# Kernel tuning notes

Measured on AMD Instinct MI355X. Metric: run time of the kernel, lower is better.

The kernel has to match this reference:

```python
import jax, jax.numpy as jnp
import numpy as np

D_MODEL = 1024
N_HEADS = 16
HEAD_DIM = D_MODEL // N_HEADS
ROPE_BASE = 10000.0


def setup_inputs() -> dict:
    key = jax.random.key(0)
    ks = jax.random.split(key, 5)
    B, S = 4, 2048
    bound_qkv = 1.0 / np.sqrt(D_MODEL)
    bound_out = 1.0 / np.sqrt(D_MODEL)
    return {
        "query": jax.random.normal(ks[0], (B, S, D_MODEL), dtype=jnp.float32),
        "W_qkv": jax.random.uniform(ks[1], (3 * D_MODEL, D_MODEL), jnp.float32, -bound_qkv, bound_qkv),
        "b_qkv": jax.random.uniform(ks[2], (3 * D_MODEL,), jnp.float32, -bound_qkv, bound_qkv),
        "W_out": jax.random.uniform(ks[3], (D_MODEL, D_MODEL), jnp.float32, -bound_out, bound_out),
        "b_out": jax.random.uniform(ks[4], (D_MODEL,), jnp.float32, -bound_out, bound_out),
    }


def _rope(x):
    # x: [B, H, S, Dh]; rotate-half RoPE, full rotational fraction
    S, Dh = x.shape[2], x.shape[3]
    half = Dh // 2
    inv_freq = 1.0 / (ROPE_BASE ** (jnp.arange(0, half, dtype=jnp.float32) * 2.0 / Dh))
    ang = jnp.arange(S, dtype=jnp.float32)[:, None] * inv_freq[None, :]  # [S, half]
    cos = jnp.concatenate([jnp.cos(ang), jnp.cos(ang)], axis=-1)  # [S, Dh]
    sin = jnp.concatenate([jnp.sin(ang), jnp.sin(ang)], axis=-1)
    x1, x2 = x[..., :half], x[..., half:]
    rot = jnp.concatenate([-x2, x1], axis=-1)
    return x * cos + rot * sin


def reference(query, W_qkv, b_qkv, W_out, b_out):
    B, S, _ = query.shape
    qkv = query @ W_qkv.T + b_qkv  # [B, S, 3*D]
    qkv = qkv.reshape(B, S, 3, N_HEADS, HEAD_DIM).transpose(2, 0, 3, 1, 4)  # [3, B, H, S, Dh]
    q, k, v = qkv[0], qkv[1], qkv[2]
    q = _rope(q)
    k = _rope(k)
    scale = 1.0 / np.sqrt(HEAD_DIM)
    scores = jnp.einsum("bhsd,bhtd->bhst", q, k) * scale  # [B, H, S, S]
    attn = jax.nn.softmax(scores, axis=-1)
    out = jnp.einsum("bhst,bhtd->bhsd", attn, v)  # [B, H, S, Dh]
    out = out.transpose(0, 2, 1, 3).reshape(B, S, D_MODEL)
    return out @ W_out.T + b_out
```

## Files before the change

kernel.cpp:

```cpp
#include <hip/hip_runtime.h>
#include <math.h>

#define D_MODEL 1024
#define N_HEADS 16
#define HEAD_DIM 64
#define BATCH 4
#define SEQ 2048
#define TOKENS (BATCH * SEQ)

typedef _Float16 f16;
typedef f16 f16x8_t __attribute__((ext_vector_type(8)));
typedef f16 f16x4_t __attribute__((ext_vector_type(4)));
typedef float f32x4_t __attribute__((ext_vector_type(4)));

#define QSCALE 0.18033688011112042f

__device__ __forceinline__ void stage16(const f16* g, f16* l) {
    __builtin_amdgcn_global_load_lds(
        (__attribute__((address_space(1))) void*)g,
        (__attribute__((address_space(3))) void*)l, 16, 0, 0);
}

__global__ void rope_table_kernel(float* __restrict__ cosT, float* __restrict__ sinT) {
    int idx = blockIdx.x * blockDim.x + threadIdx.x;
    int s = idx >> 5;
    int i = idx & 31;
    double t = (double)(2 * i) / 64.0;
    double invf = pow(10000.0, -t);
    double ang = (double)s * invf;
    cosT[idx] = (float)cos(ang);
    sinT[idx] = (float)sin(ang);
}

#define N_X  (TOKENS * D_MODEL / 4)
#define N_WQ (3 * D_MODEL * D_MODEL / 4)
#define N_WO (D_MODEL * D_MODEL / 4)
__global__ void convert_all_kernel(const float* __restrict__ X,
                                   const float* __restrict__ Wq,
                                   const float* __restrict__ Wo,
                                   f16* __restrict__ Xf, f16* __restrict__ Wqf,
                                   f16* __restrict__ Wof) {
    int i = blockIdx.x * blockDim.x + threadIdx.x;
    const float* src;
    f16* dst;
    int j;
    if (i < N_X)             { src = X;  dst = Xf;  j = i; }
    else if (i < N_X + N_WQ) { src = Wq; dst = Wqf; j = i - N_X; }
    else                     { src = Wo; dst = Wof; j = i - N_X - N_WQ; }
    float4 x = ((const float4*)src)[j];
    f16x4_t h;
    h[0] = (f16)x.x; h[1] = (f16)x.y; h[2] = (f16)x.z; h[3] = (f16)x.w;
    ((f16x4_t*)dst)[j] = h;
}

__device__ __forceinline__ void gemm_mainloop(
    const f16* __restrict__ A, const f16* __restrict__ B,
    int n0, int c0, f16* As, f16* Bs, f32x4_t acc[4][4]) {
    const int tid = threadIdx.x;
    const int lane = tid & 63;
    const int wave = tid >> 6;
    const int m16 = lane & 15, quad = lane >> 4;
    const int wm = (wave & 1) * 64, wn = (wave >> 1) * 64;

    const int srow = lane >> 3;
    const int scol = (lane & 7) << 3;

#pragma unroll
    for (int i = 0; i < 4; i++)
#pragma unroll
        for (int j = 0; j < 4; j++) acc[i][j] = (f32x4_t){0.f, 0.f, 0.f, 0.f};

    f16* ldsA = As + (wave * 32) * 64;
    f16* ldsB = Bs + (wave * 32) * 64;
    const f16* ga = A + (size_t)(n0 + wave * 32 + srow) * D_MODEL + scol;
    const f16* gb = B + (size_t)(c0 + wave * 32 + srow) * D_MODEL + scol;

    for (int kt = 0; kt < 16; kt++) {
        const int ko = kt * 64;
        __syncthreads();
#pragma unroll
        for (int inst = 0; inst < 4; inst++) {
            stage16(ga + ko + (size_t)(inst * 8) * D_MODEL, ldsA + inst * 8 * 64);
            stage16(gb + ko + (size_t)(inst * 8) * D_MODEL, ldsB + inst * 8 * 64);
        }
        __syncthreads();
#pragma unroll
        for (int kk = 0; kk < 2; kk++) {
            f16x8_t a[4], b[4];
#pragma unroll
            for (int mt = 0; mt < 4; mt++)
                a[mt] = *(const f16x8_t*)&As[(wm + mt * 16 + m16) * 64 + kk * 32 + quad * 8];
#pragma unroll
            for (int nt = 0; nt < 4; nt++)
                b[nt] = *(const f16x8_t*)&Bs[(wn + nt * 16 + m16) * 64 + kk * 32 + quad * 8];
#pragma unroll
            for (int mt = 0; mt < 4; mt++)
#pragma unroll
                for (int nt = 0; nt < 4; nt++)
                    acc[mt][nt] = __builtin_amdgcn_mfma_f32_16x16x32_f16(
                        a[mt], b[nt], acc[mt][nt], 0, 0, 0);
        }
    }
}

__global__ __launch_bounds__(256)
void qkv_gemm_kernel(const f16* __restrict__ Xf, const f16* __restrict__ Wf,
                     const float* __restrict__ bias,
                     f16* __restrict__ Qb, f16* __restrict__ Kb,
                     f16* __restrict__ VbT,
                     const float* __restrict__ cosT, const float* __restrict__ sinT) {
    __shared__ f16 As[128 * 64];
    __shared__ f16 Bs[128 * 64];
    f32x4_t acc[4][4];
    const int n0 = blockIdx.y * 128;
    const int c0 = blockIdx.x * 128;
    gemm_mainloop(Xf, Wf, n0, c0, As, Bs, acc);

    const int lane = threadIdx.x & 63;
    const int wave = threadIdx.x >> 6;
    const int m16 = lane & 15, quad = lane >> 4;
    const int wm = (wave & 1) * 64, wn = (wave >> 1) * 64;

    const int w = c0 >> 10;
    const int hh = ((c0 + wn) & 1023) >> 6;
    const int b = n0 >> 11;

    float bias4[4];
#pragma unroll
    for (int nt = 0; nt < 4; nt++) bias4[nt] = bias[c0 + wn + nt * 16 + m16];

    if (w == 2) {
        f16* vbase = VbT + ((size_t)(b * N_HEADS + hh) * HEAD_DIM) * SEQ;
#pragma unroll
        for (int mt = 0; mt < 4; mt++) {
            const int sb = (n0 + wm + mt * 16 + quad * 4) & (SEQ - 1);
#pragma unroll
            for (int nt = 0; nt < 4; nt++) {
                const int dh = nt * 16 + m16;
                f16x4_t v4;
#pragma unroll
                for (int i = 0; i < 4; i++) v4[i] = (f16)(acc[mt][nt][i] + bias4[nt]);
                *(f16x4_t*)&vbase[(size_t)dh * SEQ + sb] = v4;
            }
        }
        return;
    }

    f16* dst = (w == 0) ? Qb : Kb;
#pragma unroll
    for (int mt = 0; mt < 4; mt++)
#pragma unroll
        for (int i = 0; i < 4; i++) {
            const int n = n0 + wm + mt * 16 + quad * 4 + i;
            const int s = n & (SEQ - 1);
            f16* drow = dst + ((size_t)(b * N_HEADS + hh) * SEQ + s) * HEAD_DIM;
            float vv[4];
#pragma unroll
            for (int nt = 0; nt < 4; nt++) vv[nt] = acc[mt][nt][i] + bias4[nt];
            const float cs0 = cosT[(s << 5) + m16];
            const float sn0 = sinT[(s << 5) + m16];
            const float cs1 = cosT[(s << 5) + 16 + m16];
            const float sn1 = sinT[(s << 5) + 16 + m16];
#pragma unroll
            for (int nt = 0; nt < 4; nt++) {
                const int dh = nt * 16 + m16;
                const float cs = (nt & 1) ? cs1 : cs0;
                const float sn = (nt & 1) ? sn1 : sn0;
                const float part = vv[nt ^ 2];
                float outv = (nt >= 2) ? fmaf(vv[nt], cs, part * sn)
                                       : fmaf(vv[nt], cs, -part * sn);
                if (w == 0) outv *= QSCALE;
                drow[dh] = (f16)outv;
            }
        }
}

__global__ __launch_bounds__(256)
void out_gemm_kernel(const f16* __restrict__ Of, const f16* __restrict__ Wf,
                     const float* __restrict__ bias, float* __restrict__ Cout) {
    __shared__ f16 As[128 * 64];
    __shared__ f16 Bs[128 * 64];
    f32x4_t acc[4][4];
    const int n0 = blockIdx.y * 128;
    const int c0 = blockIdx.x * 128;
    gemm_mainloop(Of, Wf, n0, c0, As, Bs, acc);

    const int lane = threadIdx.x & 63;
    const int wave = threadIdx.x >> 6;
    const int m16 = lane & 15, quad = lane >> 4;
    const int wm = (wave & 1) * 64, wn = (wave >> 1) * 64;

    float bias4[4];
#pragma unroll
    for (int nt = 0; nt < 4; nt++) bias4[nt] = bias[c0 + wn + nt * 16 + m16];

#pragma unroll
    for (int mt = 0; mt < 4; mt++)
#pragma unroll
        for (int i = 0; i < 4; i++) {
            const int n = n0 + wm + mt * 16 + quad * 4 + i;
            float* orow = Cout + (size_t)n * D_MODEL + c0 + wn;
#pragma unroll
            for (int nt = 0; nt < 4; nt++)
                orow[nt * 16 + m16] = acc[mt][nt][i] + bias4[nt];
        }
}

#define KSW(row, g) ((g) ^ ((row) & 7))
__global__ __launch_bounds__(256, 2)
void attn_kernel(const f16* __restrict__ Qb, const f16* __restrict__ Kb,
                 const f16* __restrict__ VbT, f16* __restrict__ Of) {
    __shared__ f16 Ks[64 * 64];
    __shared__ f16 Vs[64 * 64];
    __shared__ f16 Ps[4][64][72];

    const int tid  = threadIdx.x;
    const int lane = tid & 63;
    const int wave = tid >> 6;
    const int m16  = lane & 15;
    const int quad = lane >> 4;

    const int bh = blockIdx.x & 63;
    const int qt = blockIdx.x >> 6;
    const int s0 = qt * 256;

    const f16* Kbase  = Kb + (size_t)bh * SEQ * HEAD_DIM;
    const f16* VtBase = VbT + (size_t)bh * HEAD_DIM * SEQ;

    f16x8_t bq[4][2];
#pragma unroll
    for (int nq = 0; nq < 4; nq++) {
        const f16* qrow = Qb + ((size_t)bh * SEQ + s0 + wave * 64 + nq * 16 + m16)
                          * HEAD_DIM + quad * 8;
        bq[nq][0] = *(const f16x8_t*)(qrow);
        bq[nq][1] = *(const f16x8_t*)(qrow + 32);
    }

    f32x4_t Oc[4][4];
#pragma unroll
    for (int mt = 0; mt < 4; mt++)
#pragma unroll
        for (int nq = 0; nq < 4; nq++) Oc[mt][nq] = (f32x4_t){0.f, 0.f, 0.f, 0.f};
    float sumacc[4] = {0.f, 0.f, 0.f, 0.f};

    const int lrow0 = wave * 16 + (lane >> 3);
    const int lrow1 = lrow0 + 8;
    const int gK0 = lrow0 * HEAD_DIM + KSW(lrow0, lane & 7) * 8;
    const int gK1 = lrow1 * HEAD_DIM + KSW(lrow1, lane & 7) * 8;
    const int gV0 = lrow0 * SEQ + KSW(lrow0, lane & 7) * 8;
    const int gV1 = lrow1 * SEQ + KSW(lrow1, lane & 7) * 8;
    f16* ldsK0 = Ks + (wave * 16) * 64;
    f16* ldsK1 = Ks + (wave * 16 + 8) * 64;
    f16* ldsV0 = Vs + (wave * 16) * 64;
    f16* ldsV1 = Vs + (wave * 16 + 8) * 64;

    for (int kt = 0; kt < SEQ / 64; kt++) {
        __syncthreads();
        const f16* kg = Kbase + (size_t)kt * 64 * HEAD_DIM;
        const f16* vg = VtBase + kt * 64;
        stage16(kg + gK0, ldsK0);
        stage16(kg + gK1, ldsK1);
        stage16(vg + gV0, ldsV0);
        stage16(vg + gV1, ldsV1);
        __syncthreads();

        f32x4_t Sc[4][4];
#pragma unroll
        for (int nt = 0; nt < 4; nt++)
#pragma unroll
            for (int nq = 0; nq < 4; nq++) Sc[nt][nq] = (f32x4_t){0.f, 0.f, 0.f, 0.f};
#pragma unroll
        for (int kki = 0; kki < 2; kki++) {
#pragma unroll
            for (int nt = 0; nt < 4; nt++) {
                const int row = nt * 16 + m16;
                f16x8_t ak = *(const f16x8_t*)&Ks[row * 64 + KSW(row, kki * 4 + quad) * 8];
#pragma unroll
                for (int nq = 0; nq < 4; nq++)
                    Sc[nt][nq] = __builtin_amdgcn_mfma_f32_16x16x32_f16(
                        ak, bq[nq][kki], Sc[nt][nq], 0, 0, 0);
            }
        }

#pragma unroll
        for (int nt = 0; nt < 4; nt++)
#pragma unroll
            for (int nq = 0; nq < 4; nq++) {
                f16x4_t pk4;
#pragma unroll
                for (int i = 0; i < 4; i++) {
                    float p = __builtin_amdgcn_exp2f(Sc[nt][nq][i]);
                    sumacc[nq] += p;
                    pk4[i] = (f16)p;
                }
                *(f16x4_t*)&Ps[wave][nq * 16 + m16][nt * 16 + quad * 4] = pk4;
            }

#pragma unroll
        for (int kki = 0; kki < 2; kki++) {
            f16x8_t bp[4];
#pragma unroll
            for (int nq = 0; nq < 4; nq++)
                bp[nq] = *(const f16x8_t*)&Ps[wave][nq * 16 + m16][kki * 32 + quad * 8];
#pragma unroll
            for (int mt = 0; mt < 4; mt++) {
                const int d = mt * 16 + m16;
                f16x8_t av = *(const f16x8_t*)&Vs[d * 64 + KSW(d, kki * 4 + quad) * 8];
#pragma unroll
                for (int nq = 0; nq < 4; nq++)
                    Oc[mt][nq] = __builtin_amdgcn_mfma_f32_16x16x32_f16(
                        av, bp[nq], Oc[mt][nq], 0, 0, 0);
            }
        }
    }

    const int b = bh >> 4, h = bh & 15;
#pragma unroll
    for (int nq = 0; nq < 4; nq++) {
        float l = sumacc[nq];
        l += __shfl_xor(l, 16);
        l += __shfl_xor(l, 32);
        const float invl = 1.0f / l;
        const int s = s0 + wave * 64 + nq * 16 + m16;
        const size_t off = ((size_t)(b * SEQ + s)) * D_MODEL + h * HEAD_DIM;
#pragma unroll
        for (int mt = 0; mt < 4; mt++) {
            f16x4_t o4;
#pragma unroll
            for (int i = 0; i < 4; i++)
                o4[i] = (f16)(Oc[mt][nq][i] * invl);
            *(f16x4_t*)&Of[off + mt * 16 + quad * 4] = o4;
        }
    }
}

extern "C" void kernel_launch(void* const* d_in, const int* in_sizes, int n_in,
                              void* d_out, int out_size, void* d_ws, size_t ws_size,
                              hipStream_t stream) {
    const float* X    = (const float*)d_in[0];
    const float* Wqkv = (const float*)d_in[1];
    const float* bqkv = (const float*)d_in[2];
    const float* Wout = (const float*)d_in[3];
    const float* bout = (const float*)d_in[4];
    float* out = (float*)d_out;

    char* w8 = (char*)d_ws;
    const size_t MB = 1024 * 1024;
    f16* Xf  = (f16*)(w8);
    f16* Wqf = (f16*)(w8 + 16 * MB);
    f16* Wof = (f16*)(w8 + 22 * MB);
    f16* Qf  = (f16*)(w8 + 24 * MB);
    f16* Kf  = (f16*)(w8 + 40 * MB);
    f16* VfT = (f16*)(w8 + 56 * MB);
    f16* Of  = (f16*)(w8 + 72 * MB);
    float* cosT = (float*)(w8 + 88 * MB);
    float* sinT = cosT + SEQ * 32;

    rope_table_kernel<<<(SEQ * 32) / 256, 256, 0, stream>>>(cosT, sinT);
    convert_all_kernel<<<(N_X + N_WQ + N_WO) / 256, 256, 0, stream>>>(
        X, Wqkv, Wout, Xf, Wqf, Wof);

    qkv_gemm_kernel<<<dim3(3 * D_MODEL / 128, TOKENS / 128), 256, 0, stream>>>(
        Xf, Wqf, bqkv, Qf, Kf, VfT, cosT, sinT);
    attn_kernel<<<64 * (SEQ / 256), 256, 0, stream>>>(Qf, Kf, VfT, Of);
    out_gemm_kernel<<<dim3(D_MODEL / 128, TOKENS / 128), 256, 0, stream>>>(
        Of, Wof, bout, out);
}
```

Measured before the change: 295.8 us.

## Double-buffer K/V tiles in attention and merge rope table into prep kernel

The attention kernel now keeps two K/V LDS buffers and issues the async global-to-LDS loads for the next tile before computing on the current one. This replaces the two barriers per iteration with one waitcnt plus barrier at the end of the loop. MFMA groups are wrapped in s_setprio to favour matrix issue. The rope table generation is folded into the conversion kernel to save a launch. The cost is doubled K/V LDS, which may reduce occupancy at two blocks per CU.

```diff
diff --git a/kernel.cpp b/kernel.cpp
--- a/kernel.cpp
+++ b/kernel.cpp
@@ -21,26 +21,28 @@
         (__attribute__((address_space(3))) void*)l, 16, 0, 0);
 }
 
-__global__ void rope_table_kernel(float* __restrict__ cosT, float* __restrict__ sinT) {
-    int idx = blockIdx.x * blockDim.x + threadIdx.x;
-    int s = idx >> 5;
-    int i = idx & 31;
-    double t = (double)(2 * i) / 64.0;
-    double invf = pow(10000.0, -t);
-    double ang = (double)s * invf;
-    cosT[idx] = (float)cos(ang);
-    sinT[idx] = (float)sin(ang);
-}
-
 #define N_X  (TOKENS * D_MODEL / 4)
 #define N_WQ (3 * D_MODEL * D_MODEL / 4)
 #define N_WO (D_MODEL * D_MODEL / 4)
-__global__ void convert_all_kernel(const float* __restrict__ X,
-                                   const float* __restrict__ Wq,
-                                   const float* __restrict__ Wo,
-                                   f16* __restrict__ Xf, f16* __restrict__ Wqf,
-                                   f16* __restrict__ Wof) {
+#define N_CONV (N_X + N_WQ + N_WO)
+__global__ void prep_kernel(const float* __restrict__ X,
+                            const float* __restrict__ Wq,
+                            const float* __restrict__ Wo,
+                            f16* __restrict__ Xf, f16* __restrict__ Wqf,
+                            f16* __restrict__ Wof,
+                            float* __restrict__ cosT, float* __restrict__ sinT) {
     int i = blockIdx.x * blockDim.x + threadIdx.x;
+    if (i >= N_CONV) {
+        int idx = i - N_CONV;
+        int s = idx >> 5;
+        int ii = idx & 31;
+        double t = (double)(2 * ii) / 64.0;
+        double invf = pow(10000.0, -t);
+        double ang = (double)s * invf;
+        cosT[idx] = (float)cos(ang);
+        sinT[idx] = (float)sin(ang);
+        return;
+    }
     const float* src;
     f16* dst;
     int j;
@@ -207,11 +209,12 @@
 }
 
 #define KSW(row, g) ((g) ^ ((row) & 7))
+#define NT (SEQ / 64)
 __global__ __launch_bounds__(256, 2)
 void attn_kernel(const f16* __restrict__ Qb, const f16* __restrict__ Kb,
                  const f16* __restrict__ VbT, f16* __restrict__ Of) {
-    __shared__ f16 Ks[64 * 64];
-    __shared__ f16 Vs[64 * 64];
+    __shared__ f16 Ks[2][64 * 64];
+    __shared__ f16 Vs[2][64 * 64];
     __shared__ f16 Ps[4][64][72];
 
     const int tid  = threadIdx.x;
@@ -249,20 +252,33 @@
     const int gK1 = lrow1 * HEAD_DIM + KSW(lrow1, lane & 7) * 8;
     const int gV0 = lrow0 * SEQ + KSW(lrow0, lane & 7) * 8;
     const int gV1 = lrow1 * SEQ + KSW(lrow1, lane & 7) * 8;
-    f16* ldsK0 = Ks + (wave * 16) * 64;
-    f16* ldsK1 = Ks + (wave * 16 + 8) * 64;
-    f16* ldsV0 = Vs + (wave * 16) * 64;
-    f16* ldsV1 = Vs + (wave * 16 + 8) * 64;
-
-    for (int kt = 0; kt < SEQ / 64; kt++) {
-        __syncthreads();
-        const f16* kg = Kbase + (size_t)kt * 64 * HEAD_DIM;
-        const f16* vg = VtBase + kt * 64;
-        stage16(kg + gK0, ldsK0);
-        stage16(kg + gK1, ldsK1);
-        stage16(vg + gV0, ldsV0);
-        stage16(vg + gV1, ldsV1);
-        __syncthreads();
+    const int lO0 = (wave * 16) * 64;
+    const int lO1 = (wave * 16 + 8) * 64;
+
+    stage16(Kbase + gK0, &Ks[0][lO0]);
+    stage16(Kbase + gK1, &Ks[0][lO1]);
+    stage16(VtBase + gV0, &Vs[0][lO0]);
+    stage16(VtBase + gV1, &Vs[0][lO1]);
+    asm volatile("s_waitcnt vmcnt(0)" ::: "memory");
+    __builtin_amdgcn_s_barrier();
+    asm volatile("" ::: "memory");
+
+    for (int kt = 0; kt < NT; kt++) {
+        const int cur = kt & 1;
+
+        if (kt + 1 < NT) {
+            const f16* kg = Kbase + (size_t)(kt + 1) * 64 * HEAD_DIM;
+            const f16* vg = VtBase + (kt + 1) * 64;
+            f16* kd = &Ks[cur ^ 1][0];
+            f16* vd = &Vs[cur ^ 1][0];
+            stage16(kg + gK0, kd + lO0);
+            stage16(kg + gK1, kd + lO1);
+            stage16(vg + gV0, vd + lO0);
+            stage16(vg + gV1, vd + lO1);
+        }
+
+        const f16* Kc = &Ks[cur][0];
+        const f16* Vc = &Vs[cur][0];
 
         f32x4_t Sc[4][4];
 #pragma unroll
@@ -274,11 +290,13 @@
 #pragma unroll
             for (int nt = 0; nt < 4; nt++) {
                 const int row = nt * 16 + m16;
-                f16x8_t ak = *(const f16x8_t*)&Ks[row * 64 + KSW(row, kki * 4 + quad) * 8];
+                f16x8_t ak = *(const f16x8_t*)&Kc[row * 64 + KSW(row, kki * 4 + quad) * 8];
+                __builtin_amdgcn_s_setprio(1);
 #pragma unroll
                 for (int nq = 0; nq < 4; nq++)
                     Sc[nt][nq] = __builtin_amdgcn_mfma_f32_16x16x32_f16(
                         ak, bq[nq][kki], Sc[nt][nq], 0, 0, 0);
+                __builtin_amdgcn_s_setprio(0);
             }
         }
 
@@ -305,13 +323,19 @@
 #pragma unroll
             for (int mt = 0; mt < 4; mt++) {
                 const int d = mt * 16 + m16;
-                f16x8_t av = *(const f16x8_t*)&Vs[d * 64 + KSW(d, kki * 4 + quad) * 8];
+                f16x8_t av = *(const f16x8_t*)&Vc[d * 64 + KSW(d, kki * 4 + quad) * 8];
+                __builtin_amdgcn_s_setprio(1);
 #pragma unroll
                 for (int nq = 0; nq < 4; nq++)
                     Oc[mt][nq] = __builtin_amdgcn_mfma_f32_16x16x32_f16(
                         av, bp[nq], Oc[mt][nq], 0, 0, 0);
-            }
-        }
+                __builtin_amdgcn_s_setprio(0);
+            }
+        }
+
+        asm volatile("s_waitcnt vmcnt(0)" ::: "memory");
+        __builtin_amdgcn_s_barrier();
+        asm volatile("" ::: "memory");
     }
 
     const int b = bh >> 4, h = bh & 15;
@@ -356,9 +380,8 @@
     float* cosT = (float*)(w8 + 88 * MB);
     float* sinT = cosT + SEQ * 32;
 
-    rope_table_kernel<<<(SEQ * 32) / 256, 256, 0, stream>>>(cosT, sinT);
-    convert_all_kernel<<<(N_X + N_WQ + N_WO) / 256, 256, 0, stream>>>(
-        X, Wqkv, Wout, Xf, Wqf, Wof);
+    prep_kernel<<<(N_CONV + SEQ * 32) / 256, 256, 0, stream>>>(
+        X, Wqkv, Wout, Xf, Wqf, Wof, cosT, sinT);
 
     qkv_gemm_kernel<<<dim3(3 * D_MODEL / 128, TOKENS / 128), 256, 0, stream>>>(
         Xf, Wqf, bqkv, Qf, Kf, VfT, cosT, sinT);
```

Result: no change. 296.9 us (+0.4%).
